# Performance work log

Measured on AMD Instinct MI355X. Metric: run time of the kernel, lower is better.

The kernel has to match this reference:

```python
import jax, jax.numpy as jnp
import numpy as np

NUM_HEADS = 16


def setup_inputs() -> dict:
    key = jax.random.key(0)
    ks = jax.random.split(key, 9)
    B, S, C = 2, 2048, 1024
    s = 1.0 / np.sqrt(C)
    return {
        "hidden_states": jax.random.normal(ks[0], (B, S, C), jnp.float32),
        "Wq": jax.random.normal(ks[1], (C, C), jnp.float32) * s,
        "bq": jnp.zeros((C,), jnp.float32),
        "Wk": jax.random.normal(ks[2], (C, C), jnp.float32) * s,
        "bk": jnp.zeros((C,), jnp.float32),
        "Wv": jax.random.normal(ks[3], (C, C), jnp.float32) * s,
        "bv": jnp.zeros((C,), jnp.float32),
        "Wo": jax.random.normal(ks[4], (C, C), jnp.float32) * s,
        "bo": jnp.zeros((C,), jnp.float32),
    }


def reference(hidden_states, Wq, bq, Wk, bk, Wv, bv, Wo, bo):
    # Self-attention path of AttnProcessor (3D input, no mask, no norms,
    # residual_connection=True, rescale_output_factor=1.0).
    B, S, C = hidden_states.shape
    H = NUM_HEADS
    D = C // H
    residual = hidden_states

    q = hidden_states @ Wq + bq  # [B,S,C]
    k = hidden_states @ Wk + bk
    v = hidden_states @ Wv + bv

    # head_to_batch_dim: [B,S,C] -> [B,S,H,D]
    q = q.reshape(B, S, H, D)
    k = k.reshape(B, S, H, D)
    v = v.reshape(B, S, H, D)

    scale = 1.0 / np.sqrt(D).astype(np.float32)
    # get_attention_scores: baddbmm with scale, then softmax (full [B,H,S,S])
    scores = jnp.einsum("bqhd,bkhd->bhqk", q, k) * scale
    probs = jax.nn.softmax(scores, axis=-1)

    out = jnp.einsum("bhqk,bkhd->bqhd", probs, v)  # bmm(probs, value)
    out = out.reshape(B, S, C)  # batch_to_head_dim

    out = out @ Wo + bo  # to_out[0]; to_out[1] is dropout (identity in eval)
    out = out + residual  # residual_connection
    return out  # rescale_output_factor = 1.0
```

## Files before the change

### kernel.cpp

```cpp
#include <hip/hip_runtime.h>

#define BATCH 2
#define SEQ   2048
#define CH    1024
#define NHEAD 16
#define HDIM  64
#define MROWS (BATCH * SEQ)

typedef __attribute__((ext_vector_type(8))) short short8;
typedef __attribute__((ext_vector_type(4))) float floatx4;
typedef unsigned short ushort_t;

__device__ __forceinline__ float b2f(ushort_t u) {
    union { unsigned int i; float f; } x;
    x.i = ((unsigned int)u) << 16;
    return x.f;
}
__device__ __forceinline__ ushort_t f2b(float f) {
    union { float f; unsigned int i; } x;
    x.f = f;
    unsigned int lsb = (x.i >> 16) & 1u;
    x.i += 0x7fffu + lsb;
    return (ushort_t)(x.i >> 16);
}

__device__ __forceinline__ void gld16(const ushort_t* g, ushort_t* l) {
    __builtin_amdgcn_global_load_lds(
        (const __attribute__((address_space(1))) void*)g,
        (__attribute__((address_space(3))) void*)l, 16, 0, 0);
}

__global__ __launch_bounds__(256) void cvt_bf16_kernel(
    const float* __restrict__ in, ushort_t* __restrict__ out, int n4) {
    int i = blockIdx.x * blockDim.x + threadIdx.x;
    if (i < n4) {
        float4 v = ((const float4*)in)[i];
        ushort4 o = {f2b(v.x), f2b(v.y), f2b(v.z), f2b(v.w)};
        ((ushort4*)out)[i] = o;
    }
}

__global__ __launch_bounds__(256) void transpose_cvt_all(
    const float* __restrict__ W0, const float* __restrict__ W1,
    const float* __restrict__ W2, const float* __restrict__ W3,
    ushort_t* __restrict__ T0, ushort_t* __restrict__ T1,
    ushort_t* __restrict__ T2, ushort_t* __restrict__ T3) {
    __shared__ ushort_t T[64][68];
    const int z = blockIdx.z;
    const float* W = (z == 0) ? W0 : (z == 1) ? W1 : (z == 2) ? W2 : W3;
    ushort_t* Wt = (z == 0) ? T0 : (z == 1) ? T1 : (z == 2) ? T2 : T3;
    const int tid = threadIdx.x;
    const int n0 = blockIdx.x * 64, k0 = blockIdx.y * 64;
    const int r = tid >> 4, c4 = (tid & 15) * 4;
#pragma unroll
    for (int p = 0; p < 4; p++) {
        int k = p * 16 + r;
        float4 v = *(const float4*)&W[(size_t)(k0 + k) * CH + n0 + c4];
        T[c4 + 0][k] = f2b(v.x);
        T[c4 + 1][k] = f2b(v.y);
        T[c4 + 2][k] = f2b(v.z);
        T[c4 + 3][k] = f2b(v.w);
    }
    __syncthreads();
#pragma unroll
    for (int p = 0; p < 4; p++) {
        int n = p * 16 + r;
        ushort4 o = {T[n][c4 + 0], T[n][c4 + 1], T[n][c4 + 2], T[n][c4 + 3]};
        *(ushort4*)&Wt[(size_t)(n0 + n) * CH + k0 + c4] = o;
    }
}

__device__ __forceinline__ void gemm_core(
    const ushort_t* __restrict__ A, const ushort_t* __restrict__ Bt,
    int bm, int n0, int tid, floatx4 acc[4][4],
    ushort_t* As, ushort_t* Bs) {
    const int wave = tid >> 6, lane = tid & 63;
    const int quad = lane >> 4, t16 = lane & 15;
    const int wm = wave >> 1, wn = wave & 1;
    const int arow = tid >> 2, ak = (tid & 3) * 8;

#pragma unroll
    for (int i = 0; i < 4; i++)
#pragma unroll
        for (int j = 0; j < 4; j++) acc[i][j] = (floatx4){0.f, 0.f, 0.f, 0.f};

    for (int k0 = 0; k0 < CH; k0 += 32) {
        __syncthreads();
        gld16(A + (size_t)(bm + arow) * CH + k0 + ak, As + wave * 512);
        gld16(A + (size_t)(bm + 64 + arow) * CH + k0 + ak, As + 2048 + wave * 512);
        gld16(Bt + (size_t)(n0 + arow) * CH + k0 + ak, Bs + wave * 512);
        gld16(Bt + (size_t)(n0 + 64 + arow) * CH + k0 + ak, Bs + 2048 + wave * 512);
        __syncthreads();

        short8 af[4], bf[4];
#pragma unroll
        for (int i = 0; i < 4; i++)
            af[i] = *(const short8*)&As[(wm * 64 + i * 16 + t16) * 32 + quad * 8];
#pragma unroll
        for (int j = 0; j < 4; j++)
            bf[j] = *(const short8*)&Bs[(wn * 64 + j * 16 + t16) * 32 + quad * 8];
#pragma unroll
        for (int i = 0; i < 4; i++)
#pragma unroll
            for (int j = 0; j < 4; j++)
                acc[i][j] = __builtin_amdgcn_mfma_f32_16x16x32_bf16(
                    af[i], bf[j], acc[i][j], 0, 0, 0);
    }
}

__global__ __launch_bounds__(256) void gemm_qkv(
    const ushort_t* __restrict__ X,
    const ushort_t* __restrict__ WqT, const ushort_t* __restrict__ WkT,
    const ushort_t* __restrict__ WvT,
    const float* __restrict__ bq, const float* __restrict__ bk,
    const float* __restrict__ bv,
    ushort_t* __restrict__ Qm, ushort_t* __restrict__ Km,
    ushort_t* __restrict__ Vtm) {
    __shared__ ushort_t As[128 * 32];
    __shared__ ushort_t Bs[128 * 32];
    const int tid = threadIdx.x;
    const int seg = blockIdx.x >> 3;
    const int n0 = (blockIdx.x & 7) * 128;
    const int bm = blockIdx.y * 128;
    const ushort_t* Bt = (seg == 0) ? WqT : (seg == 1) ? WkT : WvT;
    const float* bias = (seg == 0) ? bq : (seg == 1) ? bk : bv;

    floatx4 acc[4][4];
    gemm_core(X, Bt, bm, n0, tid, acc, As, Bs);

    const int lane = tid & 63, wave = tid >> 6;
    const int quad = lane >> 4, t16 = lane & 15;
    const int wm = wave >> 1, wn = wave & 1;

    if (seg < 2) {
        ushort_t* outp = seg ? Km : Qm;
        const float sc = seg ? 1.0f : 0.125f;
#pragma unroll
        for (int i = 0; i < 4; i++)
#pragma unroll
            for (int j = 0; j < 4; j++) {
                const int col = n0 + wn * 64 + j * 16 + t16;
                const float bb = bias[col];
                const int row0 = bm + wm * 64 + i * 16 + quad * 4;
#pragma unroll
                for (int r = 0; r < 4; r++)
                    outp[(size_t)(row0 + r) * CH + col] =
                        f2b((acc[i][j][r] + bb) * sc);
            }
    } else {
#pragma unroll
        for (int i = 0; i < 4; i++)
#pragma unroll
            for (int j = 0; j < 4; j++) {
                const int col = n0 + wn * 64 + j * 16 + t16;
                const int h = col >> 6, d = col & 63;
                const int row0 = bm + wm * 64 + i * 16 + quad * 4;
                const int b = row0 >> 11, s = row0 & (SEQ - 1);
                const float bb = bias[col];
                ushort4 o = {f2b(acc[i][j][0] + bb), f2b(acc[i][j][1] + bb),
                             f2b(acc[i][j][2] + bb), f2b(acc[i][j][3] + bb)};
                *(ushort4*)&Vtm[(((size_t)b * NHEAD + h) * HDIM + d) * SEQ + s] = o;
            }
    }
}

__global__ __launch_bounds__(256) void gemm_out(
    const ushort_t* __restrict__ Am, const ushort_t* __restrict__ WoT,
    const float* __restrict__ bo, const float* __restrict__ resid,
    float* __restrict__ out) {
    __shared__ ushort_t As[128 * 32];
    __shared__ ushort_t Bs[64 * 32];
    const int tid = threadIdx.x;
    const int n0 = blockIdx.x * 64;
    const int bm = blockIdx.y * 128;
    const int wave = tid >> 6, lane = tid & 63;
    const int quad = lane >> 4, t16 = lane & 15;
    const int arow = tid >> 2, ak = (tid & 3) * 8;

    floatx4 acc[2][4];
#pragma unroll
    for (int i = 0; i < 2; i++)
#pragma unroll
        for (int j = 0; j < 4; j++) acc[i][j] = (floatx4){0.f, 0.f, 0.f, 0.f};

    for (int k0 = 0; k0 < CH; k0 += 32) {
        __syncthreads();
        gld16(Am + (size_t)(bm + arow) * CH + k0 + ak, As + wave * 512);
        gld16(Am + (size_t)(bm + 64 + arow) * CH + k0 + ak, As + 2048 + wave * 512);
        gld16(WoT + (size_t)(n0 + arow) * CH + k0 + ak, Bs + wave * 512);
        __syncthreads();

        short8 af[2], bf[4];
#pragma unroll
        for (int i = 0; i < 2; i++)
            af[i] = *(const short8*)&As[(wave * 32 + i * 16 + t16) * 32 + quad * 8];
#pragma unroll
        for (int j = 0; j < 4; j++)
            bf[j] = *(const short8*)&Bs[(j * 16 + t16) * 32 + quad * 8];
#pragma unroll
        for (int i = 0; i < 2; i++)
#pragma unroll
            for (int j = 0; j < 4; j++)
                acc[i][j] = __builtin_amdgcn_mfma_f32_16x16x32_bf16(
                    af[i], bf[j], acc[i][j], 0, 0, 0);
    }

#pragma unroll
    for (int i = 0; i < 2; i++)
#pragma unroll
        for (int j = 0; j < 4; j++) {
            const int col = n0 + j * 16 + t16;
            const float bb = bo[col];
            const int row0 = bm + wave * 32 + i * 16 + quad * 4;
#pragma unroll
            for (int r = 0; r < 4; r++) {
                const size_t idx = (size_t)(row0 + r) * CH + col;
                out[idx] = acc[i][j][r] + bb + resid[idx];
            }
        }
}

__global__ __launch_bounds__(256, 4) void flash_attn_mfma(
    const ushort_t* __restrict__ Q, const ushort_t* __restrict__ K,
    const ushort_t* __restrict__ Vt, ushort_t* __restrict__ O) {
    __shared__ ushort_t Ks[64][72];
    __shared__ ushort_t Vs[64][72];
    __shared__ ushort_t Ps[4][32][72];

    const int tid = threadIdx.x;
    const int wave = tid >> 6, lane = tid & 63;
    const int quad = lane >> 4, t16 = lane & 15;
    const int bh = blockIdx.y, b = bh >> 4, h = bh & 15;
    const int q0 = blockIdx.x * 128;

    const size_t base_q = ((size_t)b * SEQ) * CH + (size_t)h * HDIM;
    const size_t base_vt = ((size_t)(b * NHEAD + h)) * HDIM * SEQ;

    short8 qf[2][2];
#pragma unroll
    for (int u = 0; u < 2; u++) {
        const ushort_t* qp =
            Q + base_q + (size_t)(q0 + wave * 32 + u * 16 + t16) * CH + quad * 8;
        qf[u][0] = *(const short8*)(qp);
        qf[u][1] = *(const short8*)(qp + 32);
    }

    const short8 ones = (short8)(short)0x3F80;

    floatx4 Oa[2][4];
    floatx4 Oe[2];
#pragma unroll
    for (int u = 0; u < 2; u++) {
        Oe[u] = (floatx4){0.f, 0.f, 0.f, 0.f};
#pragma unroll
        for (int d = 0; d < 4; d++) Oa[u][d] = (floatx4){0.f, 0.f, 0.f, 0.f};
    }

    const int r4 = tid >> 2;
    const int c16 = (tid & 3) * 16;

    for (int k0 = 0; k0 < SEQ; k0 += 64) {
        __syncthreads();
        {
            const ushort_t* kp = K + base_q + (size_t)(k0 + r4) * CH + c16;
            const ushort_t* vp = Vt + base_vt + (size_t)r4 * SEQ + k0 + c16;
            *(short8*)(&Ks[r4][c16]) = *(const short8*)(kp);
            *(short8*)(&Ks[r4][c16 + 8]) = *(const short8*)(kp + 8);
            *(short8*)(&Vs[r4][c16]) = *(const short8*)(vp);
            *(short8*)(&Vs[r4][c16 + 8]) = *(const short8*)(vp + 8);
        }
        __syncthreads();

#pragma unroll
        for (int j = 0; j < 4; j++) {
            short8 kf0 = *(const short8*)(&Ks[j * 16 + t16][quad * 8]);
            short8 kf1 = *(const short8*)(&Ks[j * 16 + t16][32 + quad * 8]);
#pragma unroll
            for (int u = 0; u < 2; u++) {
                floatx4 z = (floatx4){0.f, 0.f, 0.f, 0.f};
                z = __builtin_amdgcn_mfma_f32_16x16x32_bf16(qf[u][0], kf0, z, 0, 0, 0);
                z = __builtin_amdgcn_mfma_f32_16x16x32_bf16(qf[u][1], kf1, z, 0, 0, 0);
#pragma unroll
                for (int r = 0; r < 4; r++)
                    Ps[wave][u * 16 + quad * 4 + r][j * 16 + t16] =
                        f2b(__expf(z[r]));
            }
        }

        short8 pf[2][2];
#pragma unroll
        for (int u = 0; u < 2; u++) {
            pf[u][0] = *(const short8*)(&Ps[wave][u * 16 + t16][quad * 8]);
            pf[u][1] = *(const short8*)(&Ps[wave][u * 16 + t16][32 + quad * 8]);
        }
#pragma unroll
        for (int d = 0; d < 4; d++) {
            short8 vf0 = *(const short8*)(&Vs[d * 16 + t16][quad * 8]);
            short8 vf1 = *(const short8*)(&Vs[d * 16 + t16][32 + quad * 8]);
#pragma unroll
            for (int u = 0; u < 2; u++) {
                Oa[u][d] = __builtin_amdgcn_mfma_f32_16x16x32_bf16(
                    pf[u][0], vf0, Oa[u][d], 0, 0, 0);
                Oa[u][d] = __builtin_amdgcn_mfma_f32_16x16x32_bf16(
                    pf[u][1], vf1, Oa[u][d], 0, 0, 0);
            }
        }
#pragma unroll
        for (int u = 0; u < 2; u++) {
            Oe[u] = __builtin_amdgcn_mfma_f32_16x16x32_bf16(pf[u][0], ones, Oe[u], 0, 0, 0);
            Oe[u] = __builtin_amdgcn_mfma_f32_16x16x32_bf16(pf[u][1], ones, Oe[u], 0, 0, 0);
        }
    }

#pragma unroll
    for (int u = 0; u < 2; u++) {
        float inv[4];
#pragma unroll
        for (int r = 0; r < 4; r++) inv[r] = 1.f / Oe[u][r];
#pragma unroll
        for (int d = 0; d < 4; d++)
#pragma unroll
            for (int r = 0; r < 4; r++) {
                const int row = q0 + wave * 32 + u * 16 + quad * 4 + r;
                O[base_q + (size_t)row * CH + d * 16 + t16] =
                    f2b(Oa[u][d][r] * inv[r]);
            }
    }
}

extern "C" void kernel_launch(void* const* d_in, const int* in_sizes, int n_in,
                              void* d_out, int out_size, void* d_ws,
                              size_t ws_size, hipStream_t stream) {
    const float* X  = (const float*)d_in[0];
    const float* Wq = (const float*)d_in[1];
    const float* bq = (const float*)d_in[2];
    const float* Wk = (const float*)d_in[3];
    const float* bk = (const float*)d_in[4];
    const float* Wv = (const float*)d_in[5];
    const float* bv = (const float*)d_in[6];
    const float* Wo = (const float*)d_in[7];
    const float* bo = (const float*)d_in[8];
    float* out = (float*)d_out;

    const size_t MC = (size_t)MROWS * CH;
    const size_t WC = (size_t)CH * CH;
    ushort_t* ws  = (ushort_t*)d_ws;
    ushort_t* X16 = ws;
    ushort_t* Am  = ws;
    ushort_t* Qm  = ws + MC;
    ushort_t* Km  = ws + 2 * MC;
    ushort_t* Vtm = ws + 3 * MC;
    ushort_t* WqT = ws + 4 * MC;
    ushort_t* WkT = ws + 4 * MC + WC;
    ushort_t* WvT = ws + 4 * MC + 2 * WC;
    ushort_t* WoT = ws + 4 * MC + 3 * WC;

    dim3 blk(256);

    cvt_bf16_kernel<<<dim3((MC / 4 + 255) / 256), blk, 0, stream>>>(X, X16, (int)(MC / 4));
    transpose_cvt_all<<<dim3(16, 16, 4), blk, 0, stream>>>(
        Wq, Wk, Wv, Wo, WqT, WkT, WvT, WoT);

    gemm_qkv<<<dim3(24, 32), blk, 0, stream>>>(X16, WqT, WkT, WvT, bq, bk, bv,
                                               Qm, Km, Vtm);

    flash_attn_mfma<<<dim3(SEQ / 128, BATCH * NHEAD), blk, 0, stream>>>(Qm, Km, Vtm, Am);

    gemm_out<<<dim3(16, 32), blk, 0, stream>>>(Am, WoT, bo, X, out);
}
```

Before: 222.3 us.

## Keep attention probabilities in registers via shuffles and double K-step in GEMMs

Result: no change. 225.1 us (+1.3%).

```diff
diff --git a/kernel.cpp b/kernel.cpp
--- a/kernel.cpp
+++ b/kernel.cpp
@@ -22,6 +22,9 @@
     unsigned int lsb = (x.i >> 16) & 1u;
     x.i += 0x7fffu + lsb;
     return (ushort_t)(x.i >> 16);
+}
+__device__ __forceinline__ unsigned pack2(float a, float b) {
+    return (unsigned)f2b(a) | ((unsigned)f2b(b) << 16);
 }
 
 __device__ __forceinline__ void gld16(const ushort_t* g, ushort_t* l) {
@@ -72,8 +75,11 @@
 
 __device__ __forceinline__ void gemm_core(
     const ushort_t* __restrict__ A, const ushort_t* __restrict__ Bt,
-    int bm, int n0, int tid, floatx4 acc[4][4],
-    ushort_t* As, ushort_t* Bs) {
+    int bm, int n0, int tid, floatx4 acc[4][4], ushort_t* lds) {
+    ushort_t* As0 = lds;
+    ushort_t* As1 = lds + 4096;
+    ushort_t* Bs0 = lds + 8192;
+    ushort_t* Bs1 = lds + 12288;
     const int wave = tid >> 6, lane = tid & 63;
     const int quad = lane >> 4, t16 = lane & 15;
     const int wm = wave >> 1, wn = wave & 1;
@@ -84,27 +90,36 @@
 #pragma unroll
         for (int j = 0; j < 4; j++) acc[i][j] = (floatx4){0.f, 0.f, 0.f, 0.f};
 
-    for (int k0 = 0; k0 < CH; k0 += 32) {
-        __syncthreads();
-        gld16(A + (size_t)(bm + arow) * CH + k0 + ak, As + wave * 512);
-        gld16(A + (size_t)(bm + 64 + arow) * CH + k0 + ak, As + 2048 + wave * 512);
-        gld16(Bt + (size_t)(n0 + arow) * CH + k0 + ak, Bs + wave * 512);
-        gld16(Bt + (size_t)(n0 + 64 + arow) * CH + k0 + ak, Bs + 2048 + wave * 512);
-        __syncthreads();
-
-        short8 af[4], bf[4];
-#pragma unroll
-        for (int i = 0; i < 4; i++)
-            af[i] = *(const short8*)&As[(wm * 64 + i * 16 + t16) * 32 + quad * 8];
-#pragma unroll
-        for (int j = 0; j < 4; j++)
-            bf[j] = *(const short8*)&Bs[(wn * 64 + j * 16 + t16) * 32 + quad * 8];
-#pragma unroll
-        for (int i = 0; i < 4; i++)
+    for (int k0 = 0; k0 < CH; k0 += 64) {
+        __syncthreads();
+        gld16(A + (size_t)(bm + arow) * CH + k0 + ak, As0 + wave * 512);
+        gld16(A + (size_t)(bm + 64 + arow) * CH + k0 + ak, As0 + 2048 + wave * 512);
+        gld16(A + (size_t)(bm + arow) * CH + k0 + 32 + ak, As1 + wave * 512);
+        gld16(A + (size_t)(bm + 64 + arow) * CH + k0 + 32 + ak, As1 + 2048 + wave * 512);
+        gld16(Bt + (size_t)(n0 + arow) * CH + k0 + ak, Bs0 + wave * 512);
+        gld16(Bt + (size_t)(n0 + 64 + arow) * CH + k0 + ak, Bs0 + 2048 + wave * 512);
+        gld16(Bt + (size_t)(n0 + arow) * CH + k0 + 32 + ak, Bs1 + wave * 512);
+        gld16(Bt + (size_t)(n0 + 64 + arow) * CH + k0 + 32 + ak, Bs1 + 2048 + wave * 512);
+        __syncthreads();
+
+#pragma unroll
+        for (int kk = 0; kk < 2; kk++) {
+            const ushort_t* Ak = kk ? As1 : As0;
+            const ushort_t* Bk = kk ? Bs1 : Bs0;
+            short8 af[4], bf[4];
+#pragma unroll
+            for (int i = 0; i < 4; i++)
+                af[i] = *(const short8*)&Ak[(wm * 64 + i * 16 + t16) * 32 + quad * 8];
 #pragma unroll
             for (int j = 0; j < 4; j++)
-                acc[i][j] = __builtin_amdgcn_mfma_f32_16x16x32_bf16(
-                    af[i], bf[j], acc[i][j], 0, 0, 0);
+                bf[j] = *(const short8*)&Bk[(wn * 64 + j * 16 + t16) * 32 + quad * 8];
+#pragma unroll
+            for (int i = 0; i < 4; i++)
+#pragma unroll
+                for (int j = 0; j < 4; j++)
+                    acc[i][j] = __builtin_amdgcn_mfma_f32_16x16x32_bf16(
+                        af[i], bf[j], acc[i][j], 0, 0, 0);
+        }
     }
 }
 
@@ -116,8 +131,7 @@
     const float* __restrict__ bv,
     ushort_t* __restrict__ Qm, ushort_t* __restrict__ Km,
     ushort_t* __restrict__ Vtm) {
-    __shared__ ushort_t As[128 * 32];
-    __shared__ ushort_t Bs[128 * 32];
+    __shared__ ushort_t lds[4 * 4096];
     const int tid = threadIdx.x;
     const int seg = blockIdx.x >> 3;
     const int n0 = (blockIdx.x & 7) * 128;
@@ -126,7 +140,7 @@
     const float* bias = (seg == 0) ? bq : (seg == 1) ? bk : bv;
 
     floatx4 acc[4][4];
-    gemm_core(X, Bt, bm, n0, tid, acc, As, Bs);
+    gemm_core(X, Bt, bm, n0, tid, acc, lds);
 
     const int lane = tid & 63, wave = tid >> 6;
     const int quad = lane >> 4, t16 = lane & 15;
@@ -168,8 +182,11 @@
     const ushort_t* __restrict__ Am, const ushort_t* __restrict__ WoT,
     const float* __restrict__ bo, const float* __restrict__ resid,
     float* __restrict__ out) {
-    __shared__ ushort_t As[128 * 32];
-    __shared__ ushort_t Bs[64 * 32];
+    __shared__ ushort_t lds[2 * 4096 + 2 * 2048];
+    ushort_t* As0 = lds;
+    ushort_t* As1 = lds + 4096;
+    ushort_t* Bs0 = lds + 8192;
+    ushort_t* Bs1 = lds + 10240;
     const int tid = threadIdx.x;
     const int n0 = blockIdx.x * 64;
     const int bm = blockIdx.y * 128;
@@ -183,26 +200,34 @@
 #pragma unroll
         for (int j = 0; j < 4; j++) acc[i][j] = (floatx4){0.f, 0.f, 0.f, 0.f};
 
-    for (int k0 = 0; k0 < CH; k0 += 32) {
-        __syncthreads();
-        gld16(Am + (size_t)(bm + arow) * CH + k0 + ak, As + wave * 512);
-        gld16(Am + (size_t)(bm + 64 + arow) * CH + k0 + ak, As + 2048 + wave * 512);
-        gld16(WoT + (size_t)(n0 + arow) * CH + k0 + ak, Bs + wave * 512);
-        __syncthreads();
-
-        short8 af[2], bf[4];
-#pragma unroll
-        for (int i = 0; i < 2; i++)
-            af[i] = *(const short8*)&As[(wave * 32 + i * 16 + t16) * 32 + quad * 8];
-#pragma unroll
-        for (int j = 0; j < 4; j++)
-            bf[j] = *(const short8*)&Bs[(j * 16 + t16) * 32 + quad * 8];
-#pragma unroll
-        for (int i = 0; i < 2; i++)
+    for (int k0 = 0; k0 < CH; k0 += 64) {
+        __syncthreads();
+        gld16(Am + (size_t)(bm + arow) * CH + k0 + ak, As0 + wave * 512);
+        gld16(Am + (size_t)(bm + 64 + arow) * CH + k0 + ak, As0 + 2048 + wave * 512);
+        gld16(Am + (size_t)(bm + arow) * CH + k0 + 32 + ak, As1 + wave * 512);
+        gld16(Am + (size_t)(bm + 64 + arow) * CH + k0 + 32 + ak, As1 + 2048 + wave * 512);
+        gld16(WoT + (size_t)(n0 + arow) * CH + k0 + ak, Bs0 + wave * 512);
+        gld16(WoT + (size_t)(n0 + arow) * CH + k0 + 32 + ak, Bs1 + wave * 512);
+        __syncthreads();
+
+#pragma unroll
+        for (int kk = 0; kk < 2; kk++) {
+            const ushort_t* Ak = kk ? As1 : As0;
+            const ushort_t* Bk = kk ? Bs1 : Bs0;
+            short8 af[2], bf[4];
+#pragma unroll
+            for (int i = 0; i < 2; i++)
+                af[i] = *(const short8*)&Ak[(wave * 32 + i * 16 + t16) * 32 + quad * 8];
 #pragma unroll
             for (int j = 0; j < 4; j++)
-                acc[i][j] = __builtin_amdgcn_mfma_f32_16x16x32_bf16(
-                    af[i], bf[j], acc[i][j], 0, 0, 0);
+                bf[j] = *(const short8*)&Bk[(j * 16 + t16) * 32 + quad * 8];
+#pragma unroll
+            for (int i = 0; i < 2; i++)
+#pragma unroll
+                for (int j = 0; j < 4; j++)
+                    acc[i][j] = __builtin_amdgcn_mfma_f32_16x16x32_bf16(
+                        af[i], bf[j], acc[i][j], 0, 0, 0);
+        }
     }
 
 #pragma unroll
@@ -220,12 +245,11 @@
         }
 }
 
-__global__ __launch_bounds__(256, 4) void flash_attn_mfma(
+__global__ __launch_bounds__(256) void flash_attn_mfma(
     const ushort_t* __restrict__ Q, const ushort_t* __restrict__ K,
     const ushort_t* __restrict__ Vt, ushort_t* __restrict__ O) {
     __shared__ ushort_t Ks[64][72];
     __shared__ ushort_t Vs[64][72];
-    __shared__ ushort_t Ps[4][32][72];
 
     const int tid = threadIdx.x;
     const int wave = tid >> 6, lane = tid & 63;
@@ -258,6 +282,7 @@
 
     const int r4 = tid >> 2;
     const int c16 = (tid & 3) * 16;
+    const int qh = quad >> 1, ql = quad & 1;
 
     for (int k0 = 0; k0 < SEQ; k0 += 64) {
         __syncthreads();
@@ -271,60 +296,64 @@
         }
         __syncthreads();
 
-#pragma unroll
-        for (int j = 0; j < 4; j++) {
-            short8 kf0 = *(const short8*)(&Ks[j * 16 + t16][quad * 8]);
-            short8 kf1 = *(const short8*)(&Ks[j * 16 + t16][32 + quad * 8]);
-#pragma unroll
-            for (int u = 0; u < 2; u++) {
+        short8 kf[4][2], vf[4][2];
+#pragma unroll
+        for (int kt = 0; kt < 4; kt++) {
+            kf[kt][0] = *(const short8*)(&Ks[kt * 16 + t16][quad * 8]);
+            kf[kt][1] = *(const short8*)(&Ks[kt * 16 + t16][32 + quad * 8]);
+            vf[kt][0] = *(const short8*)(&Vs[kt * 16 + t16][quad * 8]);
+            vf[kt][1] = *(const short8*)(&Vs[kt * 16 + t16][32 + quad * 8]);
+        }
+
+#pragma unroll
+        for (int u = 0; u < 2; u++) {
+            unsigned pk[4][2];
+#pragma unroll
+            for (int kt = 0; kt < 4; kt++) {
                 floatx4 z = (floatx4){0.f, 0.f, 0.f, 0.f};
-                z = __builtin_amdgcn_mfma_f32_16x16x32_bf16(qf[u][0], kf0, z, 0, 0, 0);
-                z = __builtin_amdgcn_mfma_f32_16x16x32_bf16(qf[u][1], kf1, z, 0, 0, 0);
-#pragma unroll
-                for (int r = 0; r < 4; r++)
-                    Ps[wave][u * 16 + quad * 4 + r][j * 16 + t16] =
-                        f2b(__expf(z[r]));
-            }
-        }
-
-        short8 pf[2][2];
-#pragma unroll
-        for (int u = 0; u < 2; u++) {
-            pf[u][0] = *(const short8*)(&Ps[wave][u * 16 + t16][quad * 8]);
-            pf[u][1] = *(const short8*)(&Ps[wave][u * 16 + t16][32 + quad * 8]);
-        }
-#pragma unroll
-        for (int d = 0; d < 4; d++) {
-            short8 vf0 = *(const short8*)(&Vs[d * 16 + t16][quad * 8]);
-            short8 vf1 = *(const short8*)(&Vs[d * 16 + t16][32 + quad * 8]);
-#pragma unroll
-            for (int u = 0; u < 2; u++) {
-                Oa[u][d] = __builtin_amdgcn_mfma_f32_16x16x32_bf16(
-                    pf[u][0], vf0, Oa[u][d], 0, 0, 0);
-                Oa[u][d] = __builtin_amdgcn_mfma_f32_16x16x32_bf16(
-                    pf[u][1], vf1, Oa[u][d], 0, 0, 0);
-            }
-        }
-#pragma unroll
-        for (int u = 0; u < 2; u++) {
-            Oe[u] = __builtin_amdgcn_mfma_f32_16x16x32_bf16(pf[u][0], ones, Oe[u], 0, 0, 0);
-            Oe[u] = __builtin_amdgcn_mfma_f32_16x16x32_bf16(pf[u][1], ones, Oe[u], 0, 0, 0);
+                z = __builtin_amdgcn_mfma_f32_16x16x32_bf16(kf[kt][0], qf[u][0], z, 0, 0, 0);
+                z = __builtin_amdgcn_mfma_f32_16x16x32_bf16(kf[kt][1], qf[u][1], z, 0, 0, 0);
+                pk[kt][0] = pack2(__expf(z[0]), __expf(z[1]));
+                pk[kt][1] = pack2(__expf(z[2]), __expf(z[3]));
+            }
+            short8 pf[2];
+#pragma unroll
+            for (int kb = 0; kb < 2; kb++) {
+                unsigned dw[4];
+#pragma unroll
+                for (int dp = 0; dp < 4; dp++) {
+                    const int src = ((ql * 2 + (dp >> 1)) << 4) + t16;
+                    unsigned lo = __shfl(pk[kb * 2 + 0][dp & 1], src);
+                    unsigned hi = __shfl(pk[kb * 2 + 1][dp & 1], src);
+                    dw[dp] = qh ? hi : lo;
+                }
+                union { unsigned u32[4]; short8 s8; } cvt;
+                cvt.u32[0] = dw[0]; cvt.u32[1] = dw[1];
+                cvt.u32[2] = dw[2]; cvt.u32[3] = dw[3];
+                pf[kb] = cvt.s8;
+            }
+#pragma unroll
+            for (int kb = 0; kb < 2; kb++) {
+#pragma unroll
+                for (int dt = 0; dt < 4; dt++)
+                    Oa[u][dt] = __builtin_amdgcn_mfma_f32_16x16x32_bf16(
+                        vf[dt][kb], pf[kb], Oa[u][dt], 0, 0, 0);
+                Oe[u] = __builtin_amdgcn_mfma_f32_16x16x32_bf16(
+                    ones, pf[kb], Oe[u], 0, 0, 0);
+            }
         }
     }
 
 #pragma unroll
     for (int u = 0; u < 2; u++) {
-        float inv[4];
-#pragma unroll
-        for (int r = 0; r < 4; r++) inv[r] = 1.f / Oe[u][r];
-#pragma unroll
-        for (int d = 0; d < 4; d++)
-#pragma unroll
-            for (int r = 0; r < 4; r++) {
-                const int row = q0 + wave * 32 + u * 16 + quad * 4 + r;
-                O[base_q + (size_t)row * CH + d * 16 + t16] =
-                    f2b(Oa[u][d][r] * inv[r]);
-            }
+        const float inv = 1.f / Oe[u][0];
+        const int row = q0 + wave * 32 + u * 16 + t16;
+#pragma unroll
+        for (int dt = 0; dt < 4; dt++) {
+            ushort4 o = {f2b(Oa[u][dt][0] * inv), f2b(Oa[u][dt][1] * inv),
+                         f2b(Oa[u][dt][2] * inv), f2b(Oa[u][dt][3] * inv)};
+            *(ushort4*)&O[base_q + (size_t)row * CH + dt * 16 + quad * 4] = o;
+        }
     }
 }
 
```

## Double-buffer LDS in projection GEMMs and stage V transpose through LDS

Applied to the files above, without the earlier changes.

New measurement: 217.1 us. 2.3% less time.

```diff
diff --git a/kernel.cpp b/kernel.cpp
--- a/kernel.cpp
+++ b/kernel.cpp
@@ -22,6 +22,9 @@
     unsigned int lsb = (x.i >> 16) & 1u;
     x.i += 0x7fffu + lsb;
     return (ushort_t)(x.i >> 16);
+}
+__device__ __forceinline__ unsigned pack2(float a, float b) {
+    return (unsigned)f2b(a) | ((unsigned)f2b(b) << 16);
 }
 
 __device__ __forceinline__ void gld16(const ushort_t* g, ushort_t* l) {
@@ -70,28 +73,37 @@
     }
 }
 
-__device__ __forceinline__ void gemm_core(
+__device__ __forceinline__ void gemm_core_db(
     const ushort_t* __restrict__ A, const ushort_t* __restrict__ Bt,
-    int bm, int n0, int tid, floatx4 acc[4][4],
-    ushort_t* As, ushort_t* Bs) {
+    int bm, int n0, int tid, floatx4 acc[4][4], ushort_t* lds) {
     const int wave = tid >> 6, lane = tid & 63;
     const int quad = lane >> 4, t16 = lane & 15;
     const int wm = wave >> 1, wn = wave & 1;
     const int arow = tid >> 2, ak = (tid & 3) * 8;
 
+    const ushort_t* a0 = A + (size_t)(bm + arow) * CH + ak;
+    const ushort_t* a1 = A + (size_t)(bm + 64 + arow) * CH + ak;
+    const ushort_t* b0 = Bt + (size_t)(n0 + arow) * CH + ak;
+    const ushort_t* b1 = Bt + (size_t)(n0 + 64 + arow) * CH + ak;
+
 #pragma unroll
     for (int i = 0; i < 4; i++)
 #pragma unroll
         for (int j = 0; j < 4; j++) acc[i][j] = (floatx4){0.f, 0.f, 0.f, 0.f};
 
-    for (int k0 = 0; k0 < CH; k0 += 32) {
+    {
+        ushort_t* As = lds;
+        ushort_t* Bs = lds + 4096;
+        gld16(a0, As + wave * 512);
+        gld16(a1, As + 2048 + wave * 512);
+        gld16(b0, Bs + wave * 512);
+        gld16(b1, Bs + 2048 + wave * 512);
+    }
+
+    for (int it = 0; it < CH / 32; ++it) {
         __syncthreads();
-        gld16(A + (size_t)(bm + arow) * CH + k0 + ak, As + wave * 512);
-        gld16(A + (size_t)(bm + 64 + arow) * CH + k0 + ak, As + 2048 + wave * 512);
-        gld16(Bt + (size_t)(n0 + arow) * CH + k0 + ak, Bs + wave * 512);
-        gld16(Bt + (size_t)(n0 + 64 + arow) * CH + k0 + ak, Bs + 2048 + wave * 512);
-        __syncthreads();
-
+        const ushort_t* As = lds + (it & 1) * 8192;
+        const ushort_t* Bs = As + 4096;
         short8 af[4], bf[4];
 #pragma unroll
         for (int i = 0; i < 4; i++)
@@ -99,6 +111,15 @@
 #pragma unroll
         for (int j = 0; j < 4; j++)
             bf[j] = *(const short8*)&Bs[(wn * 64 + j * 16 + t16) * 32 + quad * 8];
+        if (it + 1 < CH / 32) {
+            ushort_t* nAs = lds + ((it + 1) & 1) * 8192;
+            ushort_t* nBs = nAs + 4096;
+            const int k = (it + 1) * 32;
+            gld16(a0 + k, nAs + wave * 512);
+            gld16(a1 + k, nAs + 2048 + wave * 512);
+            gld16(b0 + k, nBs + wave * 512);
+            gld16(b1 + k, nBs + 2048 + wave * 512);
+        }
 #pragma unroll
         for (int i = 0; i < 4; i++)
 #pragma unroll
@@ -116,8 +137,7 @@
     const float* __restrict__ bv,
     ushort_t* __restrict__ Qm, ushort_t* __restrict__ Km,
     ushort_t* __restrict__ Vtm) {
-    __shared__ ushort_t As[128 * 32];
-    __shared__ ushort_t Bs[128 * 32];
+    __shared__ ushort_t lds[2 * 8192];
     const int tid = threadIdx.x;
     const int seg = blockIdx.x >> 3;
     const int n0 = (blockIdx.x & 7) * 128;
@@ -126,7 +146,7 @@
     const float* bias = (seg == 0) ? bq : (seg == 1) ? bk : bv;
 
     floatx4 acc[4][4];
-    gemm_core(X, Bt, bm, n0, tid, acc, As, Bs);
+    gemm_core_db(X, Bt, bm, n0, tid, acc, lds);
 
     const int lane = tid & 63, wave = tid >> 6;
     const int quad = lane >> 4, t16 = lane & 15;
@@ -148,19 +168,37 @@
                         f2b((acc[i][j][r] + bb) * sc);
             }
     } else {
-#pragma unroll
-        for (int i = 0; i < 4; i++)
-#pragma unroll
-            for (int j = 0; j < 4; j++) {
-                const int col = n0 + wn * 64 + j * 16 + t16;
-                const int h = col >> 6, d = col & 63;
-                const int row0 = bm + wm * 64 + i * 16 + quad * 4;
-                const int b = row0 >> 11, s = row0 & (SEQ - 1);
-                const float bb = bias[col];
-                ushort4 o = {f2b(acc[i][j][0] + bb), f2b(acc[i][j][1] + bb),
-                             f2b(acc[i][j][2] + bb), f2b(acc[i][j][3] + bb)};
-                *(ushort4*)&Vtm[(((size_t)b * NHEAD + h) * HDIM + d) * SEQ + s] = o;
-            }
+        ushort_t* rep = lds;
+        const int b = bm >> 11;
+        const int s_base = bm & (SEQ - 1);
+#pragma unroll
+        for (int half = 0; half < 2; half++) {
+            __syncthreads();
+            if (wn == half) {
+#pragma unroll
+                for (int i = 0; i < 4; i++)
+#pragma unroll
+                    for (int j = 0; j < 4; j++) {
+                        const int dl = j * 16 + t16;
+                        const int sl = wm * 64 + i * 16 + quad * 4;
+                        const float bb = bias[n0 + half * 64 + dl];
+                        uint2 w = {pack2(acc[i][j][0] + bb, acc[i][j][1] + bb),
+                                   pack2(acc[i][j][2] + bb, acc[i][j][3] + bb)};
+                        *(uint2*)&rep[dl * 136 + sl] = w;
+                    }
+            }
+            __syncthreads();
+#pragma unroll
+            for (int step = 0; step < 4; step++) {
+                const int dl = step * 16 + (tid >> 4);
+                const int sl = (tid & 15) * 8;
+                short8 v = *(const short8*)&rep[dl * 136 + sl];
+                const int col = n0 + half * 64 + dl;
+                const int h = col >> 6, dd = col & 63;
+                *(short8*)&Vtm[(((size_t)b * NHEAD + h) * HDIM + dd) * SEQ +
+                               s_base + sl] = v;
+            }
+        }
     }
 }
 
@@ -168,8 +206,7 @@
     const ushort_t* __restrict__ Am, const ushort_t* __restrict__ WoT,
     const float* __restrict__ bo, const float* __restrict__ resid,
     float* __restrict__ out) {
-    __shared__ ushort_t As[128 * 32];
-    __shared__ ushort_t Bs[64 * 32];
+    __shared__ ushort_t lds[2 * 6144];
     const int tid = threadIdx.x;
     const int n0 = blockIdx.x * 64;
     const int bm = blockIdx.y * 128;
@@ -177,19 +214,26 @@
     const int quad = lane >> 4, t16 = lane & 15;
     const int arow = tid >> 2, ak = (tid & 3) * 8;
 
+    const ushort_t* a0 = Am + (size_t)(bm + arow) * CH + ak;
+    const ushort_t* a1 = Am + (size_t)(bm + 64 + arow) * CH + ak;
+    const ushort_t* b0 = WoT + (size_t)(n0 + arow) * CH + ak;
+
     floatx4 acc[2][4];
 #pragma unroll
     for (int i = 0; i < 2; i++)
 #pragma unroll
         for (int j = 0; j < 4; j++) acc[i][j] = (floatx4){0.f, 0.f, 0.f, 0.f};
 
-    for (int k0 = 0; k0 < CH; k0 += 32) {
+    {
+        gld16(a0, lds + wave * 512);
+        gld16(a1, lds + 2048 + wave * 512);
+        gld16(b0, lds + 4096 + wave * 512);
+    }
+
+    for (int it = 0; it < CH / 32; ++it) {
         __syncthreads();
-        gld16(Am + (size_t)(bm + arow) * CH + k0 + ak, As + wave * 512);
-        gld16(Am + (size_t)(bm + 64 + arow) * CH + k0 + ak, As + 2048 + wave * 512);
-        gld16(WoT + (size_t)(n0 + arow) * CH + k0 + ak, Bs + wave * 512);
-        __syncthreads();
-
+        const ushort_t* As = lds + (it & 1) * 6144;
+        const ushort_t* Bs = As + 4096;
         short8 af[2], bf[4];
 #pragma unroll
         for (int i = 0; i < 2; i++)
@@ -197,6 +241,13 @@
 #pragma unroll
         for (int j = 0; j < 4; j++)
             bf[j] = *(const short8*)&Bs[(j * 16 + t16) * 32 + quad * 8];
+        if (it + 1 < CH / 32) {
+            ushort_t* nAs = lds + ((it + 1) & 1) * 6144;
+            const int k = (it + 1) * 32;
+            gld16(a0 + k, nAs + wave * 512);
+            gld16(a1 + k, nAs + 2048 + wave * 512);
+            gld16(b0 + k, nAs + 4096 + wave * 512);
+        }
 #pragma unroll
         for (int i = 0; i < 2; i++)
 #pragma unroll
```
